# Kernel tuning notes

Hardware: AMD Instinct MI355X
Metric: run time of the kernel (lower is better)

## Reference

```python
import jax, jax.numpy as jnp
import numpy as np

BATCH = 16      # self.batch_size
EPS = 1e-5      # BatchNorm2d default eps


def setup_inputs() -> dict:
    key = jax.random.key(0)
    ks = jax.random.split(key, 8)
    inp = {
        # mailbox['agg_feat']: [total_nodes = B*npoints, K, C_in] = [16384, 64, 67]
        'agg_feat': jax.random.normal(ks[0], (16384, 64, 67), jnp.float32),
        # layer 0: Conv2d(67, 64, 1) + BN(64)
        'w0': jax.random.normal(ks[1], (64, 67), jnp.float32) * 0.1,
        'b0': jnp.zeros((64,), jnp.float32),
        'g0': jnp.ones((64,), jnp.float32),
        'be0': jnp.zeros((64,), jnp.float32),
        # layer 1: Conv2d(64, 64, 1) + BN(64)
        'w1': jax.random.normal(ks[2], (64, 64), jnp.float32) * 0.1,
        'b1': jnp.zeros((64,), jnp.float32),
        'g1': jnp.ones((64,), jnp.float32),
        'be1': jnp.zeros((64,), jnp.float32),
        # layer 2: Conv2d(64, 128, 1) + BN(128)
        'w2': jax.random.normal(ks[3], (128, 64), jnp.float32) * 0.1,
        'b2': jnp.zeros((128,), jnp.float32),
        'g2': jnp.ones((128,), jnp.float32),
        'be2': jnp.zeros((128,), jnp.float32),
    }
    return inp


def _conv_bn_relu(h, w, b, g, be):
    # 1x1 Conv2d on NCHW: contraction over input channels only
    h = jnp.einsum('oc,bcnk->bonk', w, h) + b[None, :, None, None]
    # BatchNorm2d in training mode: biased batch stats over (B, N, K) per channel
    mean = jnp.mean(h, axis=(0, 2, 3), keepdims=True)
    var = jnp.mean(jnp.square(h - mean), axis=(0, 2, 3), keepdims=True)
    h = (h - mean) * jax.lax.rsqrt(var + EPS)
    h = h * g[None, :, None, None] + be[None, :, None, None]
    return jax.nn.relu(h)


def reference(agg_feat, w0, b0, g0, be0, w1, b1, g1, be1, w2, b2, g2, be2):
    total, K, C = agg_feat.shape
    npoints = total // BATCH
    # [total, K, C] -> [B, npoints, K, C] -> [B, C, npoints, K]
    h = agg_feat.reshape(BATCH, npoints, K, C).transpose(0, 3, 1, 2)
    for w, b, g, be in ((w0, b0, g0, be0), (w1, b1, g1, be1), (w2, b2, g2, be2)):
        h = _conv_bn_relu(h, w, b, g, be)
    # max over neighbor axis K -> [B, C_out, npoints]
    h = jnp.max(h, axis=3)
    feat_dim = h.shape[1]
    # [B, C_out, npoints] -> [B, npoints, C_out] -> [B*npoints, C_out]
    return h.transpose(0, 2, 1).reshape(-1, feat_dim)
```

## Files before the change

### kernel.cpp

```cpp
#include <hip/hip_runtime.h>

#define ROWS  16384
#define PTOT  1048576
#define NTOTF 1048576.0f
#define EPSF  1e-5f
#define NREP  16

typedef _Float16 half8  __attribute__((ext_vector_type(8)));
typedef _Float16 half2v __attribute__((ext_vector_type(2)));
typedef __fp16   fp16x2 __attribute__((ext_vector_type(2)));
typedef __attribute__((ext_vector_type(4))) float floatx4;
typedef float f32x4 __attribute__((ext_vector_type(4)));
typedef f32x4 f32x4u __attribute__((aligned(4)));

union H8 { half8 v8; half2v v2[4]; };
union PK2 { fp16x2 p; half2v h; unsigned int u; };

__device__ __forceinline__ half2v cvt2(float lo, float hi) {
    PK2 k; k.p = __builtin_amdgcn_cvt_pkrtz(lo, hi); return k.h;
}
__device__ __forceinline__ unsigned int cvt2u(float lo, float hi) {
    PK2 k; k.p = __builtin_amdgcn_cvt_pkrtz(lo, hi); return k.u;
}
__device__ __forceinline__ float relu_f(float x) { return x > 0.f ? x : 0.f; }

__device__ __forceinline__ half8 h8zero() {
    half8 z = {(_Float16)0.f, (_Float16)0.f, (_Float16)0.f, (_Float16)0.f,
               (_Float16)0.f, (_Float16)0.f, (_Float16)0.f, (_Float16)0.f};
    return z;
}

__device__ __forceinline__ half2v bn2(half2v h, half2v a, half2v b) {
    half2v z = {(_Float16)0.f, (_Float16)0.f};
    return __builtin_elementwise_max((half2v)(h * a + b), z);
}

__global__ __launch_bounds__(256) void k_conv0(
    const float* __restrict__ X, const float* __restrict__ w0,
    const float* __restrict__ b0, _Float16* __restrict__ H,
    float* __restrict__ stats)
{
    __shared__ float sred[64], s2red[64];
    const int tid  = threadIdx.x;
    const int lane = tid & 63;
    const int wid  = tid >> 6;
    const int ln15 = lane & 15;
    const int quad = lane >> 4;
    const int pbase = blockIdx.x * 256 + wid * 64;

    if (tid < 64) { sred[tid] = 0.f; s2red[tid] = 0.f; }
    __syncthreads();

    half8 afr[4][3];
    floatx4 bias[4];
#pragma unroll
    for (int mt = 0; mt < 4; ++mt) {
        const float* wr = w0 + (size_t)(mt * 16 + ln15) * 67;
#pragma unroll
        for (int kh = 0; kh < 2; ++kh) {
            f32x4u wa = *reinterpret_cast<const f32x4u*>(wr + kh * 32 + quad * 8);
            f32x4u wb = *reinterpret_cast<const f32x4u*>(wr + kh * 32 + quad * 8 + 4);
            H8 t;
            t.v2[0] = cvt2(wa[0], wa[1]);
            t.v2[1] = cvt2(wa[2], wa[3]);
            t.v2[2] = cvt2(wb[0], wb[1]);
            t.v2[3] = cvt2(wb[2], wb[3]);
            afr[mt][kh] = t.v8;
        }
        H8 t; t.v8 = h8zero();
        if (quad == 0) {
            f32x4u tv = *reinterpret_cast<const f32x4u*>(wr + 63);
            t.v2[0] = cvt2(tv[1], tv[2]);
            t.v2[1] = cvt2(tv[3], 0.f);
        }
        afr[mt][2] = t.v8;
        bias[mt] = *reinterpret_cast<const floatx4*>(b0 + mt * 16 + quad * 4);
    }

    float s[4][4] = {}, s2[4][4] = {};
#pragma unroll 2
    for (int nt = 0; nt < 4; ++nt) {
        const int pos = pbase + nt * 16 + ln15;
        const float* xr = X + (size_t)pos * 67;
        H8 B0, B1, BT;
        {
            f32x4u xa = *reinterpret_cast<const f32x4u*>(xr + quad * 8);
            f32x4u xb = *reinterpret_cast<const f32x4u*>(xr + quad * 8 + 4);
            f32x4u xc = *reinterpret_cast<const f32x4u*>(xr + 32 + quad * 8);
            f32x4u xd = *reinterpret_cast<const f32x4u*>(xr + 32 + quad * 8 + 4);
            B0.v2[0] = cvt2(xa[0], xa[1]);
            B0.v2[1] = cvt2(xa[2], xa[3]);
            B0.v2[2] = cvt2(xb[0], xb[1]);
            B0.v2[3] = cvt2(xb[2], xb[3]);
            B1.v2[0] = cvt2(xc[0], xc[1]);
            B1.v2[1] = cvt2(xc[2], xc[3]);
            B1.v2[2] = cvt2(xd[0], xd[1]);
            B1.v2[3] = cvt2(xd[2], xd[3]);
            BT.v8 = h8zero();
            if (quad == 0) {
                f32x4u tv = *reinterpret_cast<const f32x4u*>(xr + 63);
                BT.v2[0] = cvt2(tv[1], tv[2]);
                BT.v2[1] = cvt2(tv[3], 0.f);
            }
        }
#pragma unroll
        for (int mt = 0; mt < 4; ++mt) {
            floatx4 c = bias[mt];
            c = __builtin_amdgcn_mfma_f32_16x16x32_f16(afr[mt][0], B0.v8, c, 0, 0, 0);
            c = __builtin_amdgcn_mfma_f32_16x16x32_f16(afr[mt][1], B1.v8, c, 0, 0, 0);
            c = __builtin_amdgcn_mfma_f32_16x16x32_f16(afr[mt][2], BT.v8, c, 0, 0, 0);
            s[mt][0] += c[0]; s2[mt][0] += c[0] * c[0];
            s[mt][1] += c[1]; s2[mt][1] += c[1] * c[1];
            s[mt][2] += c[2]; s2[mt][2] += c[2] * c[2];
            s[mt][3] += c[3]; s2[mt][3] += c[3] * c[3];
            uint2 o;
            o.x = cvt2u(c[0], c[1]);
            o.y = cvt2u(c[2], c[3]);
            *reinterpret_cast<uint2*>(&H[(size_t)pos * 64 + mt * 16 + quad * 4]) = o;
        }
    }
#pragma unroll
    for (int mt = 0; mt < 4; ++mt)
#pragma unroll
        for (int rg = 0; rg < 4; ++rg) {
            s[mt][rg]  += __shfl_xor(s[mt][rg], 1, 64);  s[mt][rg]  += __shfl_xor(s[mt][rg], 2, 64);
            s[mt][rg]  += __shfl_xor(s[mt][rg], 4, 64);  s[mt][rg]  += __shfl_xor(s[mt][rg], 8, 64);
            s2[mt][rg] += __shfl_xor(s2[mt][rg], 1, 64); s2[mt][rg] += __shfl_xor(s2[mt][rg], 2, 64);
            s2[mt][rg] += __shfl_xor(s2[mt][rg], 4, 64); s2[mt][rg] += __shfl_xor(s2[mt][rg], 8, 64);
        }
    if (ln15 == 0) {
#pragma unroll
        for (int mt = 0; mt < 4; ++mt)
#pragma unroll
            for (int rg = 0; rg < 4; ++rg) {
                atomicAdd(&sred[mt * 16 + quad * 4 + rg], s[mt][rg]);
                atomicAdd(&s2red[mt * 16 + quad * 4 + rg], s2[mt][rg]);
            }
    }
    __syncthreads();
    const int rep = (blockIdx.x & (NREP - 1)) * 512;
    if (tid < 64) {
        unsafeAtomicAdd(&stats[rep + tid], sred[tid]);
        unsafeAtomicAdd(&stats[rep + 64 + tid], s2red[tid]);
    }
}

__global__ __launch_bounds__(256) void k_conv1(
    const _Float16* __restrict__ Hin, _Float16* __restrict__ Hout,
    const float* __restrict__ w1, const float* __restrict__ b1,
    const float* __restrict__ g0, const float* __restrict__ be0,
    float* __restrict__ stats)
{
    __shared__ float als[64], bls[64], sred[64], s2red[64];
    const int tid  = threadIdx.x;
    const int lane = tid & 63;
    const int wid  = tid >> 6;
    const int ln15 = lane & 15;
    const int quad = lane >> 4;
    const int pbase = blockIdx.x * 256 + wid * 64;

    if (tid < 64) {
        float ssum = 0.f, qsum = 0.f;
#pragma unroll
        for (int r = 0; r < NREP; ++r) { ssum += stats[r * 512 + tid]; qsum += stats[r * 512 + 64 + tid]; }
        const float mean = ssum * (1.f / NTOTF);
        const float var  = qsum * (1.f / NTOTF) - mean * mean;
        const float a    = g0[tid] / sqrtf(var + EPSF);
        als[tid] = a; bls[tid] = be0[tid] - mean * a;
        sred[tid] = 0.f; s2red[tid] = 0.f;
    }
    __syncthreads();

    half2v a2[8], b2[8];
#pragma unroll
    for (int kh = 0; kh < 2; ++kh)
#pragma unroll
        for (int j2 = 0; j2 < 4; ++j2) {
            const int c0 = kh * 32 + quad * 8 + 2 * j2;
            half2v av = {(_Float16)als[c0], (_Float16)als[c0 + 1]};
            half2v bv = {(_Float16)bls[c0], (_Float16)bls[c0 + 1]};
            a2[kh * 4 + j2] = av; b2[kh * 4 + j2] = bv;
        }

    half8 afr[4][2];
    floatx4 bias[4];
#pragma unroll
    for (int mt = 0; mt < 4; ++mt) {
        const float* wr = w1 + (size_t)(mt * 16 + ln15) * 64;
#pragma unroll
        for (int kh = 0; kh < 2; ++kh) {
            f32x4 wa = *reinterpret_cast<const f32x4*>(wr + kh * 32 + quad * 8);
            f32x4 wb = *reinterpret_cast<const f32x4*>(wr + kh * 32 + quad * 8 + 4);
            H8 t;
            t.v2[0] = cvt2(wa[0], wa[1]);
            t.v2[1] = cvt2(wa[2], wa[3]);
            t.v2[2] = cvt2(wb[0], wb[1]);
            t.v2[3] = cvt2(wb[2], wb[3]);
            afr[mt][kh] = t.v8;
        }
        bias[mt] = *reinterpret_cast<const floatx4*>(b1 + mt * 16 + quad * 4);
    }

    float s[4][4] = {}, s2[4][4] = {};
#pragma unroll 2
    for (int nt = 0; nt < 4; ++nt) {
        const int pos = pbase + nt * 16 + ln15;
        H8 r0, r1;
        r0.v8 = *reinterpret_cast<const half8*>(&Hin[(size_t)pos * 64 + quad * 8]);
        r1.v8 = *reinterpret_cast<const half8*>(&Hin[(size_t)pos * 64 + 32 + quad * 8]);
        H8 f0, f1;
#pragma unroll
        for (int j2 = 0; j2 < 4; ++j2) {
            f0.v2[j2] = bn2(r0.v2[j2], a2[j2], b2[j2]);
            f1.v2[j2] = bn2(r1.v2[j2], a2[4 + j2], b2[4 + j2]);
        }
#pragma unroll
        for (int mt = 0; mt < 4; ++mt) {
            floatx4 c = bias[mt];
            c = __builtin_amdgcn_mfma_f32_16x16x32_f16(afr[mt][0], f0.v8, c, 0, 0, 0);
            c = __builtin_amdgcn_mfma_f32_16x16x32_f16(afr[mt][1], f1.v8, c, 0, 0, 0);
            s[mt][0] += c[0]; s2[mt][0] += c[0] * c[0];
            s[mt][1] += c[1]; s2[mt][1] += c[1] * c[1];
            s[mt][2] += c[2]; s2[mt][2] += c[2] * c[2];
            s[mt][3] += c[3]; s2[mt][3] += c[3] * c[3];
            uint2 o;
            o.x = cvt2u(c[0], c[1]);
            o.y = cvt2u(c[2], c[3]);
            *reinterpret_cast<uint2*>(&Hout[(size_t)pos * 64 + mt * 16 + quad * 4]) = o;
        }
    }
#pragma unroll
    for (int mt = 0; mt < 4; ++mt)
#pragma unroll
        for (int rg = 0; rg < 4; ++rg) {
            s[mt][rg]  += __shfl_xor(s[mt][rg], 1, 64);  s[mt][rg]  += __shfl_xor(s[mt][rg], 2, 64);
            s[mt][rg]  += __shfl_xor(s[mt][rg], 4, 64);  s[mt][rg]  += __shfl_xor(s[mt][rg], 8, 64);
            s2[mt][rg] += __shfl_xor(s2[mt][rg], 1, 64); s2[mt][rg] += __shfl_xor(s2[mt][rg], 2, 64);
            s2[mt][rg] += __shfl_xor(s2[mt][rg], 4, 64); s2[mt][rg] += __shfl_xor(s2[mt][rg], 8, 64);
        }
    if (ln15 == 0) {
#pragma unroll
        for (int mt = 0; mt < 4; ++mt)
#pragma unroll
            for (int rg = 0; rg < 4; ++rg) {
                atomicAdd(&sred[mt * 16 + quad * 4 + rg], s[mt][rg]);
                atomicAdd(&s2red[mt * 16 + quad * 4 + rg], s2[mt][rg]);
            }
    }
    __syncthreads();
    const int rep = (blockIdx.x & (NREP - 1)) * 512;
    if (tid < 64) {
        unsafeAtomicAdd(&stats[rep + 128 + tid], sred[tid]);
        unsafeAtomicAdd(&stats[rep + 192 + tid], s2red[tid]);
    }
}

__global__ __launch_bounds__(256) void k_conv2(
    const _Float16* __restrict__ H, const float* __restrict__ w2,
    const float* __restrict__ b2c, const float* __restrict__ g1,
    const float* __restrict__ be1, float* __restrict__ rowmax,
    float* __restrict__ rowmin, float* __restrict__ stats)
{
    __shared__ float als[64], bls[64], sred[128], s2red[128];
    const int tid  = threadIdx.x;
    const int lane = tid & 63;
    const int wid  = tid >> 6;
    const int ln15 = lane & 15;
    const int quad = lane >> 4;
    const int r0   = blockIdx.x * 4;

    if (tid < 64) {
        float ssum = 0.f, qsum = 0.f;
#pragma unroll
        for (int r = 0; r < NREP; ++r) { ssum += stats[r * 512 + 128 + tid]; qsum += stats[r * 512 + 192 + tid]; }
        const float mean = ssum * (1.f / NTOTF);
        const float var  = qsum * (1.f / NTOTF) - mean * mean;
        const float a    = g1[tid] / sqrtf(var + EPSF);
        als[tid] = a; bls[tid] = be1[tid] - mean * a;
    }
    if (tid < 128) { sred[tid] = 0.f; s2red[tid] = 0.f; }
    __syncthreads();

    half2v a2[8], b2[8];
#pragma unroll
    for (int kh = 0; kh < 2; ++kh)
#pragma unroll
        for (int j2 = 0; j2 < 4; ++j2) {
            const int c0 = kh * 32 + quad * 8 + 2 * j2;
            half2v av = {(_Float16)als[c0], (_Float16)als[c0 + 1]};
            half2v bv = {(_Float16)bls[c0], (_Float16)bls[c0 + 1]};
            a2[kh * 4 + j2] = av; b2[kh * 4 + j2] = bv;
        }

    const int chHalf = (wid & 1) * 64;
    half8 bfr[8];
    float biasn[4];
#pragma unroll
    for (int nt = 0; nt < 4; ++nt) {
        const int n = chHalf + nt * 16 + ln15;
        biasn[nt] = b2c[n];
#pragma unroll
        for (int kh = 0; kh < 2; ++kh) {
            f32x4 wa = *reinterpret_cast<const f32x4*>(&w2[(size_t)n * 64 + kh * 32 + quad * 8]);
            f32x4 wb = *reinterpret_cast<const f32x4*>(&w2[(size_t)n * 64 + kh * 32 + quad * 8 + 4]);
            H8 t;
            t.v2[0] = cvt2(wa[0], wa[1]);
            t.v2[1] = cvt2(wa[2], wa[3]);
            t.v2[2] = cvt2(wb[0], wb[1]);
            t.v2[3] = cvt2(wb[2], wb[3]);
            bfr[nt * 2 + kh] = t.v8;
        }
    }

    float s[4] = {0, 0, 0, 0}, s2[4] = {0, 0, 0, 0};
    for (int rr = 0; rr < 2; ++rr) {
        const int prow = r0 + (wid >> 1) * 2 + rr;
        float mx[4] = {-3.4e38f, -3.4e38f, -3.4e38f, -3.4e38f};
        float mn[4] = {3.4e38f, 3.4e38f, 3.4e38f, 3.4e38f};
#pragma unroll 2
        for (int mt = 0; mt < 4; ++mt) {
            const size_t rowb = (size_t)(prow * 64 + mt * 16 + ln15) * 64;
            H8 r0f, r1f;
            r0f.v8 = *reinterpret_cast<const half8*>(&H[rowb + quad * 8]);
            r1f.v8 = *reinterpret_cast<const half8*>(&H[rowb + 32 + quad * 8]);
            H8 f0, f1;
#pragma unroll
            for (int j2 = 0; j2 < 4; ++j2) {
                f0.v2[j2] = bn2(r0f.v2[j2], a2[j2], b2[j2]);
                f1.v2[j2] = bn2(r1f.v2[j2], a2[4 + j2], b2[4 + j2]);
            }
#pragma unroll
            for (int nt = 0; nt < 4; ++nt) {
                floatx4 a = {biasn[nt], biasn[nt], biasn[nt], biasn[nt]};
                a = __builtin_amdgcn_mfma_f32_16x16x32_f16(f0.v8, bfr[nt * 2 + 0], a, 0, 0, 0);
                a = __builtin_amdgcn_mfma_f32_16x16x32_f16(f1.v8, bfr[nt * 2 + 1], a, 0, 0, 0);
#pragma unroll
                for (int rg = 0; rg < 4; ++rg) {
                    const float h = a[rg];
                    mx[nt] = fmaxf(mx[nt], h);
                    mn[nt] = fminf(mn[nt], h);
                    s[nt] += h; s2[nt] += h * h;
                }
            }
        }
#pragma unroll
        for (int nt = 0; nt < 4; ++nt) {
            mx[nt] = fmaxf(mx[nt], __shfl_xor(mx[nt], 16, 64));
            mx[nt] = fmaxf(mx[nt], __shfl_xor(mx[nt], 32, 64));
            mn[nt] = fminf(mn[nt], __shfl_xor(mn[nt], 16, 64));
            mn[nt] = fminf(mn[nt], __shfl_xor(mn[nt], 32, 64));
        }
        if (lane < 16) {
#pragma unroll
            for (int nt = 0; nt < 4; ++nt) {
                rowmax[(size_t)prow * 128 + chHalf + nt * 16 + lane] = mx[nt];
                rowmin[(size_t)prow * 128 + chHalf + nt * 16 + lane] = mn[nt];
            }
        }
    }
#pragma unroll
    for (int nt = 0; nt < 4; ++nt) {
        s[nt]  += __shfl_xor(s[nt], 16, 64);  s[nt]  += __shfl_xor(s[nt], 32, 64);
        s2[nt] += __shfl_xor(s2[nt], 16, 64); s2[nt] += __shfl_xor(s2[nt], 32, 64);
    }
    if (lane < 16) {
#pragma unroll
        for (int nt = 0; nt < 4; ++nt) {
            atomicAdd(&sred[chHalf + nt * 16 + ln15], s[nt]);
            atomicAdd(&s2red[chHalf + nt * 16 + ln15], s2[nt]);
        }
    }
    __syncthreads();
    const int rep = (blockIdx.x & (NREP - 1)) * 512;
    if (tid < 128) {
        unsafeAtomicAdd(&stats[rep + 256 + tid], sred[tid]);
        unsafeAtomicAdd(&stats[rep + 384 + tid], s2red[tid]);
    }
}

__global__ __launch_bounds__(256) void k_out(
    const float* __restrict__ rowmax, const float* __restrict__ rowmin,
    const float* __restrict__ g2, const float* __restrict__ be2,
    const float* __restrict__ stats, float* __restrict__ out)
{
    __shared__ float als[128], bls[128];
    const int tid = threadIdx.x;
    if (tid < 128) {
        float ssum = 0.f, qsum = 0.f;
#pragma unroll
        for (int r = 0; r < NREP; ++r) { ssum += stats[r * 512 + 256 + tid]; qsum += stats[r * 512 + 384 + tid]; }
        const float mean = ssum * (1.f / NTOTF);
        const float var  = qsum * (1.f / NTOTF) - mean * mean;
        const float a    = g2[tid] / sqrtf(var + EPSF);
        als[tid] = a; bls[tid] = be2[tid] - mean * a;
    }
    __syncthreads();
    const int idx = blockIdx.x * 256 + tid;
    const int o = idx & 127;
    const float a = als[o];
    const float v = (a > 0.f) ? rowmax[idx] : rowmin[idx];
    out[idx] = relu_f(a * v + bls[o]);
}

extern "C" void kernel_launch(void* const* d_in, const int* in_sizes, int n_in,
                              void* d_out, int out_size, void* d_ws, size_t ws_size,
                              hipStream_t stream)
{
    (void)in_sizes; (void)n_in; (void)out_size; (void)ws_size;
    const float* X   = (const float*)d_in[0];
    const float* w0  = (const float*)d_in[1];
    const float* b0  = (const float*)d_in[2];
    const float* g0  = (const float*)d_in[3];
    const float* be0 = (const float*)d_in[4];
    const float* w1  = (const float*)d_in[5];
    const float* b1  = (const float*)d_in[6];
    const float* g1  = (const float*)d_in[7];
    const float* be1 = (const float*)d_in[8];
    const float* w2  = (const float*)d_in[9];
    const float* b2  = (const float*)d_in[10];
    const float* g2  = (const float*)d_in[11];
    const float* be2 = (const float*)d_in[12];
    float* out = (float*)d_out;

    char* ws = (char*)d_ws;
    _Float16* H = (_Float16*)ws;
    float* rowmax = (float*)(ws + 134217728);
    float* rowmin = (float*)(ws + 134217728 + 8388608);
    float* stats  = (float*)(ws + 134217728 + 2 * 8388608);

    hipMemsetAsync(stats, 0, NREP * 512 * sizeof(float), stream);
    hipLaunchKernelGGL(k_conv0, dim3(PTOT / 256), dim3(256), 0, stream, X, w0, b0, H, stats);
    hipLaunchKernelGGL(k_conv1, dim3(PTOT / 256), dim3(256), 0, stream, H, H, w1, b1, g0, be0, stats);
    hipLaunchKernelGGL(k_conv2, dim3(ROWS / 4), dim3(256), 0, stream, H, w2, b2, g1, be1, rowmax, rowmin, stats);
    hipLaunchKernelGGL(k_out, dim3(ROWS * 128 / 256), dim3(256), 0, stream, rowmax, rowmin, g2, be2, stats, out);
}
```

Measured before the change: 600.1 us.

## Stage input tiles through LDS with async global_load_lds double buffering

All three conv kernels now copy each 16-row input tile into per-wave LDS double buffers with global_load_lds, and wait on vmcnt so the next tile loads while the current one is computed. The conv1 and conv2 buffers use an XOR swizzle to avoid LDS bank conflicts when lanes read their fragments. The goal is to hide global memory latency and replace strided uncoalesced per-lane loads with contiguous 16-byte transfers. In exchange it adds LDS usage that may lower occupancy, and it relies on hand-counted vmcnt values being correct.

```diff
diff --git a/kernel.cpp b/kernel.cpp
--- a/kernel.cpp
+++ b/kernel.cpp
@@ -35,12 +35,23 @@
     return __builtin_elementwise_max((half2v)(h * a + b), z);
 }
 
+typedef const __attribute__((address_space(1))) unsigned int* gas1;
+typedef __attribute__((address_space(3))) unsigned int* las3;
+__device__ __forceinline__ void gl16(const void* g, void* l) {
+    __builtin_amdgcn_global_load_lds((gas1)(unsigned long long)g,
+                                     (las3)(unsigned int)(unsigned long long)l,
+                                     16, 0, 0);
+}
+#define WVM(N) { asm volatile("s_waitcnt vmcnt(" #N ")" ::: "memory"); __builtin_amdgcn_sched_barrier(0); }
+#define SB __builtin_amdgcn_sched_barrier(0)
+
 __global__ __launch_bounds__(256) void k_conv0(
     const float* __restrict__ X, const float* __restrict__ w0,
     const float* __restrict__ b0, _Float16* __restrict__ H,
     float* __restrict__ stats)
 {
     __shared__ float sred[64], s2red[64];
+    __shared__ __align__(16) char xbuf[4][2][4352];
     const int tid  = threadIdx.x;
     const int lane = tid & 63;
     const int wid  = tid >> 6;
@@ -78,10 +89,21 @@
     }
 
     float s[4][4] = {}, s2[4][4] = {};
-#pragma unroll 2
-    for (int nt = 0; nt < 4; ++nt) {
+
+    auto stage = [&](int nt) {
+        SB;
+        const char* src = (const char*)X + (size_t)(pbase + nt * 16) * 268;
+        char* dst = &xbuf[wid][nt & 1][0];
+#pragma unroll
+        for (int c = 0; c < 4; ++c)
+            gl16(src + c * 1024 + lane * 16, dst + c * 1024);
+        if (lane < 12) gl16(src + 4096 + lane * 16, dst + 4096);
+        SB;
+    };
+    auto compute = [&](int nt) {
+        const char* tb = &xbuf[wid][nt & 1][0];
+        const float* xr = (const float*)(tb + ln15 * 268);
         const int pos = pbase + nt * 16 + ln15;
-        const float* xr = X + (size_t)pos * 67;
         H8 B0, B1, BT;
         {
             f32x4u xa = *reinterpret_cast<const f32x4u*>(xr + quad * 8);
@@ -98,9 +120,9 @@
             B1.v2[3] = cvt2(xd[2], xd[3]);
             BT.v8 = h8zero();
             if (quad == 0) {
-                f32x4u tv = *reinterpret_cast<const f32x4u*>(xr + 63);
-                BT.v2[0] = cvt2(tv[1], tv[2]);
-                BT.v2[1] = cvt2(tv[3], 0.f);
+                const float* tf = xr + 63;
+                BT.v2[0] = cvt2(tf[1], tf[2]);
+                BT.v2[1] = cvt2(tf[3], 0.f);
             }
         }
 #pragma unroll
@@ -118,7 +140,16 @@
             o.y = cvt2u(c[2], c[3]);
             *reinterpret_cast<uint2*>(&H[(size_t)pos * 64 + mt * 16 + quad * 4]) = o;
         }
-    }
+    };
+
+    stage(0); stage(1);
+    WVM(5);  compute(0);
+    stage(2);
+    WVM(9);  compute(1);
+    stage(3);
+    WVM(9);  compute(2);
+    WVM(4);  compute(3);
+
 #pragma unroll
     for (int mt = 0; mt < 4; ++mt)
 #pragma unroll
@@ -152,12 +183,14 @@
     float* __restrict__ stats)
 {
     __shared__ float als[64], bls[64], sred[64], s2red[64];
+    __shared__ __align__(16) char hbuf[4][2][2048];
     const int tid  = threadIdx.x;
     const int lane = tid & 63;
     const int wid  = tid >> 6;
     const int ln15 = lane & 15;
     const int quad = lane >> 4;
     const int pbase = blockIdx.x * 256 + wid * 64;
+    const int swl = (((lane & 7) ^ (lane >> 3)) << 4);
 
     if (tid < 64) {
         float ssum = 0.f, qsum = 0.f;
@@ -171,7 +204,7 @@
     }
     __syncthreads();
 
-    half2v a2[8], b2[8];
+    half2v ba2[8], bb2[8];
 #pragma unroll
     for (int kh = 0; kh < 2; ++kh)
 #pragma unroll
@@ -179,7 +212,7 @@
             const int c0 = kh * 32 + quad * 8 + 2 * j2;
             half2v av = {(_Float16)als[c0], (_Float16)als[c0 + 1]};
             half2v bv = {(_Float16)bls[c0], (_Float16)bls[c0 + 1]};
-            a2[kh * 4 + j2] = av; b2[kh * 4 + j2] = bv;
+            ba2[kh * 4 + j2] = av; bb2[kh * 4 + j2] = bv;
         }
 
     half8 afr[4][2];
@@ -202,17 +235,28 @@
     }
 
     float s[4][4] = {}, s2[4][4] = {};
-#pragma unroll 2
-    for (int nt = 0; nt < 4; ++nt) {
+
+    auto stage = [&](int nt) {
+        SB;
+        const char* base = (const char*)Hin + (size_t)(pbase + nt * 16) * 128;
+        char* dst = &hbuf[wid][nt & 1][0];
+#pragma unroll
+        for (int c = 0; c < 2; ++c)
+            gl16(base + c * 1024 + (lane >> 3) * 128 + swl, dst + c * 1024);
+        SB;
+    };
+    auto compute = [&](int nt) {
+        const char* tb = &hbuf[wid][nt & 1][0];
+        const half8* rowp = (const half8*)(tb + ln15 * 128);
         const int pos = pbase + nt * 16 + ln15;
         H8 r0, r1;
-        r0.v8 = *reinterpret_cast<const half8*>(&Hin[(size_t)pos * 64 + quad * 8]);
-        r1.v8 = *reinterpret_cast<const half8*>(&Hin[(size_t)pos * 64 + 32 + quad * 8]);
+        r0.v8 = rowp[quad ^ (ln15 & 7)];
+        r1.v8 = rowp[(4 + quad) ^ (ln15 & 7)];
         H8 f0, f1;
 #pragma unroll
         for (int j2 = 0; j2 < 4; ++j2) {
-            f0.v2[j2] = bn2(r0.v2[j2], a2[j2], b2[j2]);
-            f1.v2[j2] = bn2(r1.v2[j2], a2[4 + j2], b2[4 + j2]);
+            f0.v2[j2] = bn2(r0.v2[j2], ba2[j2], bb2[j2]);
+            f1.v2[j2] = bn2(r1.v2[j2], ba2[4 + j2], bb2[4 + j2]);
         }
 #pragma unroll
         for (int mt = 0; mt < 4; ++mt) {
@@ -228,7 +272,16 @@
             o.y = cvt2u(c[2], c[3]);
             *reinterpret_cast<uint2*>(&Hout[(size_t)pos * 64 + mt * 16 + quad * 4]) = o;
         }
-    }
+    };
+
+    stage(0); stage(1);
+    WVM(2);  compute(0);
+    stage(2);
+    WVM(6);  compute(1);
+    stage(3);
+    WVM(6);  compute(2);
+    WVM(4);  compute(3);
+
 #pragma unroll
     for (int mt = 0; mt < 4; ++mt)
 #pragma unroll
@@ -262,12 +315,14 @@
     float* __restrict__ rowmin, float* __restrict__ stats)
 {
     __shared__ float als[64], bls[64], sred[128], s2red[128];
+    __shared__ __align__(16) char vbuf[4][2][2048];
     const int tid  = threadIdx.x;
     const int lane = tid & 63;
     const int wid  = tid >> 6;
     const int ln15 = lane & 15;
     const int quad = lane >> 4;
     const int r0   = blockIdx.x * 4;
+    const int swl  = (((lane & 7) ^ (lane >> 3)) << 4);
 
     if (tid < 64) {
         float ssum = 0.f, qsum = 0.f;
@@ -281,7 +336,7 @@
     if (tid < 128) { sred[tid] = 0.f; s2red[tid] = 0.f; }
     __syncthreads();
 
-    half2v a2[8], b2[8];
+    half2v ba2[8], bb2[8];
 #pragma unroll
     for (int kh = 0; kh < 2; ++kh)
 #pragma unroll
@@ -289,7 +344,7 @@
             const int c0 = kh * 32 + quad * 8 + 2 * j2;
             half2v av = {(_Float16)als[c0], (_Float16)als[c0 + 1]};
             half2v bv = {(_Float16)bls[c0], (_Float16)bls[c0 + 1]};
-            a2[kh * 4 + j2] = av; b2[kh * 4 + j2] = bv;
+            ba2[kh * 4 + j2] = av; bb2[kh * 4 + j2] = bv;
         }
 
     const int chHalf = (wid & 1) * 64;
@@ -312,22 +367,40 @@
         }
     }
 
+    const int prowbase = r0 + (wid >> 1) * 2;
+    auto stage = [&](int t) {
+        SB;
+        const char* base = (const char*)H +
+            (size_t)((prowbase + (t >> 2)) * 64 + (t & 3) * 16) * 128;
+        char* dst = &vbuf[wid][t & 1][0];
+#pragma unroll
+        for (int c = 0; c < 2; ++c)
+            gl16(base + c * 1024 + (lane >> 3) * 128 + swl, dst + c * 1024);
+        SB;
+    };
+
     float s[4] = {0, 0, 0, 0}, s2[4] = {0, 0, 0, 0};
+    stage(0);
+#pragma unroll
     for (int rr = 0; rr < 2; ++rr) {
-        const int prow = r0 + (wid >> 1) * 2 + rr;
+        const int prow = prowbase + rr;
         float mx[4] = {-3.4e38f, -3.4e38f, -3.4e38f, -3.4e38f};
         float mn[4] = {3.4e38f, 3.4e38f, 3.4e38f, 3.4e38f};
-#pragma unroll 2
+#pragma unroll
         for (int mt = 0; mt < 4; ++mt) {
-            const size_t rowb = (size_t)(prow * 64 + mt * 16 + ln15) * 64;
+            const int t = rr * 4 + mt;
+            if (t < 7) stage(t + 1);
+            if (t == 7) { WVM(0); } else { WVM(2); }
+            const char* tb = &vbuf[wid][t & 1][0];
+            const half8* rowp = (const half8*)(tb + ln15 * 128);
             H8 r0f, r1f;
-            r0f.v8 = *reinterpret_cast<const half8*>(&H[rowb + quad * 8]);
-            r1f.v8 = *reinterpret_cast<const half8*>(&H[rowb + 32 + quad * 8]);
+            r0f.v8 = rowp[quad ^ (ln15 & 7)];
+            r1f.v8 = rowp[(4 + quad) ^ (ln15 & 7)];
             H8 f0, f1;
 #pragma unroll
             for (int j2 = 0; j2 < 4; ++j2) {
-                f0.v2[j2] = bn2(r0f.v2[j2], a2[j2], b2[j2]);
-                f1.v2[j2] = bn2(r1f.v2[j2], a2[4 + j2], b2[4 + j2]);
+                f0.v2[j2] = bn2(r0f.v2[j2], ba2[j2], bb2[j2]);
+                f1.v2[j2] = bn2(r1f.v2[j2], ba2[4 + j2], bb2[4 + j2]);
             }
 #pragma unroll
             for (int nt = 0; nt < 4; ++nt) {
```

Result: faster. 585.6 us (-2.4%).
